# Kernel tuning notes

Hardware: AMD Instinct MI355X
Metric: run time of the kernel (lower is better)

Reference implementation:

```python
import jax, jax.numpy as jnp
import numpy as np

N = 200000
D = 256          # d_node
H = 1024         # n_hidden
OUT = 4002       # n_out
L = 2001
G = 4096         # number of graphs (static)


def _linear_params(key, fan_in, fan_out):
    kw, kb = jax.random.split(key)
    s = 1.0 / np.sqrt(fan_in)
    W = jax.random.uniform(kw, (fan_in, fan_out), jnp.float32, -s, s)
    b = jax.random.uniform(kb, (fan_out,), jnp.float32, -s, s)
    return W, b


def setup_inputs() -> dict:
    key = jax.random.key(0)
    ks = jax.random.split(key, 6)
    h = jax.random.normal(ks[0], (N, D), dtype=jnp.float32)
    node_graph_index = jnp.sort(jax.random.randint(ks[1], (N,), 0, G, dtype=jnp.int32))
    W_pool, b_pool = _linear_params(ks[2], D, D)
    W1, b1 = _linear_params(ks[3], D, H)
    W2, b2 = _linear_params(ks[4], H, H)
    W3, b3 = _linear_params(ks[5], H, OUT)
    return {"h": h, "node_graph_index": node_graph_index,
            "W_pool": W_pool, "b_pool": b_pool,
            "W1": W1, "b1": b1, "W2": W2, "b2": b2, "W3": W3, "b3": b3}


def reference(h, node_graph_index, W_pool, b_pool, W1, b1, W2, b2, W3, b3):
    # attention logits per node: SiLU(W_pool h + b)   [N, D]
    att = jax.nn.silu(h @ W_pool + b_pool)
    # per-graph, per-feature softmax over nodes (segment softmax)
    att_max = jax.ops.segment_max(att, node_graph_index, num_segments=G)   # [G, D]
    att_exp = jnp.exp(att - att_max[node_graph_index])                     # [N, D]
    att_sum = jax.ops.segment_sum(att_exp, node_graph_index, num_segments=G)  # [G, D]
    att_norm = att_exp / jnp.maximum(att_sum[node_graph_index], 1e-12)     # [N, D]
    # attention-weighted pooling
    h_G = jax.ops.segment_sum(h * att_norm, node_graph_index, num_segments=G)  # [G, D]
    # output MLP (depth=2 hidden SiLU layers, plain last)
    x = jax.nn.silu(h_G @ W1 + b1)
    x = jax.nn.silu(x @ W2 + b2)
    out = x @ W3 + b3                                                      # [G, 4002]
    eps_imag = out[:, :L]
    eps_real = out[:, L:]
    return out, eps_imag, eps_real
```

## Files before the change

### kernel.cpp

```cpp
#include <hip/hip_runtime.h>
#include <cstdint>
#include <cstddef>

#define NN 200000
#define DD 256
#define HH 1024
#define OUTD 4002
#define LL 2001
#define GG 4096

#define ROWS_PB 128
#define STEPS 8
#define SLOTS_L 8
#define SLOTS_G 4

typedef unsigned short u16;
typedef short short8 __attribute__((ext_vector_type(8)));
typedef float f32x4 __attribute__((ext_vector_type(4)));

static __device__ __forceinline__ u16 f2bf(float f) {
  uint32_t u = __float_as_uint(f);
  uint32_t r = (u + 0x7FFFu + ((u >> 16) & 1u)) >> 16;
  return (u16)r;
}
static __device__ __forceinline__ float bf2f(u16 b) {
  return __uint_as_float(((uint32_t)b) << 16);
}

static __device__ __forceinline__ void gld_lds16(const void* g, void* l) {
  __builtin_amdgcn_global_load_lds((const __attribute__((address_space(1))) void*)g,
                                   (__attribute__((address_space(3))) void*)l,
                                   16, 0, 0);
}

static __device__ __forceinline__ void barrier_nodrain() {
  asm volatile("s_waitcnt lgkmcnt(0)" ::: "memory");
  __builtin_amdgcn_s_barrier();
  __builtin_amdgcn_sched_barrier(0);
}

__global__ __launch_bounds__(256) void transpose_bf16(const float* __restrict__ W,
                                                      u16* __restrict__ WT,
                                                      int K, int Nc) {
  __shared__ float tile[32][33];
  int nt = blockIdx.x * 32, kt = blockIdx.y * 32;
  int tx = threadIdx.x & 31, ty = threadIdx.x >> 5;
#pragma unroll
  for (int i = 0; i < 4; ++i) {
    int k = kt + ty + i * 8, n = nt + tx;
    tile[ty + i * 8][tx] = (k < K && n < Nc) ? W[(size_t)k * Nc + n] : 0.f;
  }
  __syncthreads();
#pragma unroll
  for (int i = 0; i < 4; ++i) {
    int n = nt + ty + i * 8, k = kt + tx;
    if (n < Nc && k < K) WT[(size_t)n * K + k] = f2bf(tile[tx][ty + i * 8]);
  }
}

__global__ void graph_offsets(const int* __restrict__ idx, int* __restrict__ offs) {
  int g = blockIdx.x * blockDim.x + threadIdx.x;
  if (g > GG) return;
  int lo = 0, hi = NN;
  while (lo < hi) {
    int mid = (lo + hi) >> 1;
    if (idx[mid] < g) lo = mid + 1; else hi = mid;
  }
  offs[g] = lo;
}

__global__ __launch_bounds__(512) void fused_pool(const float* __restrict__ h,
                                                  const u16* __restrict__ WT,
                                                  const float* __restrict__ bias,
                                                  const int* __restrict__ idx,
                                                  const int* __restrict__ offs,
                                                  float* __restrict__ PS_ss,
                                                  float* __restrict__ PS_ah) {
  __shared__ __align__(16) u16 At[2][16 * 256];
  __shared__ float accS[SLOTS_L * 128];
  __shared__ float accA[SLOTS_L * 128];
  __shared__ int lidx[ROWS_PB];

  const int tid = threadIdx.x;
  const int wave = tid >> 6, lane = tid & 63;
  const int rl = lane & 15, q = lane >> 4;
  const int half = blockIdx.x;
  const int chunk = blockIdx.y;
  const int halfbase = half * 128;
  const long row0 = (long)chunk * ROWS_PB;

  if (tid < ROWS_PB) {
    long r = row0 + tid;
    lidx[tid] = (r < NN) ? idx[r] : -1;
  }
  for (int i = tid; i < SLOTS_L * 128; i += 512) { accS[i] = 0.f; accA[i] = 0.f; }

  const int fl = wave * 16 + rl;
  const int f0 = halfbase + fl;
  short8 Bf0[8];
  {
    const u16* wp0 = WT + (size_t)f0 * 256 + q * 8;
#pragma unroll
    for (int k0 = 0; k0 < 8; ++k0)
      Bf0[k0] = *reinterpret_cast<const short8*>(wp0 + k0 * 32);
  }
  const float bv0 = bias[f0];

  const int tr = tid >> 5, te = (tid & 31) * 8;
  const int wbyte = tr * 512 + ((te * 2) ^ ((tr & 7) << 4));
  float4 pf0, pf1;
  auto issue = [&](int st) {
    long r = row0 + (long)st * 16 + tr;
    if (r >= NN) r = NN - 1;
    const float* p = h + r * 256 + te;
    pf0 = *reinterpret_cast<const float4*>(p);
    pf1 = *reinterpret_cast<const float4*>(p + 4);
  };
  auto commit = [&](int bufsel) {
    short8 w;
    w[0] = (short)f2bf(pf0.x); w[1] = (short)f2bf(pf0.y);
    w[2] = (short)f2bf(pf0.z); w[3] = (short)f2bf(pf0.w);
    w[4] = (short)f2bf(pf1.x); w[5] = (short)f2bf(pf1.y);
    w[6] = (short)f2bf(pf1.z); w[7] = (short)f2bf(pf1.w);
    *reinterpret_cast<short8*>((char*)&At[0][0] + bufsel * 8192 + wbyte) = w;
  };

  int afoff[8], hv0off[4];
#pragma unroll
  for (int k0 = 0; k0 < 8; ++k0)
    afoff[k0] = rl * 512 + ((k0 * 64 + q * 16) ^ ((rl & 7) << 4));
#pragma unroll
  for (int reg = 0; reg < 4; ++reg) {
    int rloc = q * 4 + reg;
    hv0off[reg] = rloc * 512 + ((f0 * 2) ^ ((rloc & 7) << 4));
  }

  issue(0);
  commit(0);
  issue(1);
  barrier_nodrain();

  const int gfirst = lidx[0];
  int cur = -1;
  float ss0 = 0.f, ah0 = 0.f;

#pragma unroll
  for (int st = 0; st < STEPS; ++st) {
    const char* Ab = (const char*)&At[0][0] + (st & 1) * 8192;
    short8 af[8];
#pragma unroll
    for (int k0 = 0; k0 < 8; ++k0)
      af[k0] = *reinterpret_cast<const short8*>(Ab + afoff[k0]);
    f32x4 acc0 = {0.f, 0.f, 0.f, 0.f};
#pragma unroll
    for (int k0 = 0; k0 < 8; ++k0)
      acc0 = __builtin_amdgcn_mfma_f32_16x16x32_bf16(af[k0], Bf0[k0], acc0, 0, 0, 0);
#pragma unroll
    for (int reg = 0; reg < 4; ++reg) {
      const int rloc = q * 4 + reg;
      const int gid = lidx[st * 16 + rloc];
      float z0 = acc0[reg] + bv0;
      float a0 = z0 / (1.f + __expf(-z0));
      float x0 = __expf(a0);
      float hv0 = bf2f(*reinterpret_cast<const u16*>(Ab + hv0off[reg]));
      if (gid != cur) {
        if (cur >= 0) {
          int sl = cur - gfirst; if (sl >= SLOTS_L) sl = SLOTS_L - 1;
          atomicAdd(&accS[sl * 128 + fl], ss0);
          atomicAdd(&accA[sl * 128 + fl], ah0);
        }
        ss0 = ah0 = 0.f;
        cur = gid;
      }
      if (gid >= 0) {
        ss0 += x0;
        ah0 = __builtin_fmaf(x0, hv0, ah0);
      }
    }
    if (st + 1 < STEPS) {
      commit((st + 1) & 1);
      if (st + 2 < STEPS) issue(st + 2);
    }
    barrier_nodrain();
  }

  if (cur >= 0) {
    int sl = cur - gfirst; if (sl >= SLOTS_L) sl = SLOTS_L - 1;
    atomicAdd(&accS[sl * 128 + fl], ss0);
    atomicAdd(&accA[sl * 128 + fl], ah0);
  }
  __syncthreads();

  long lastrow = row0 + ROWS_PB - 1; if (lastrow >= NN) lastrow = NN - 1;
  const int glast = idx[lastrow];
  int gspan = glast - gfirst + 1; if (gspan > SLOTS_L) gspan = SLOTS_L;
  const int f = tid & 127, which = (tid >> 7) & 1;
  for (int s = tid >> 8; s < gspan; s += 2) {
    int g = gfirst + s;
    int osl = chunk - (offs[g] >> 7);
    if (osl < 0) osl = 0;
    if (osl >= SLOTS_G) osl = SLOTS_G - 1;
    float v = which ? accA[s * 128 + f] : accS[s * 128 + f];
    float* dst = which ? PS_ah : PS_ss;
    dst[((size_t)g * SLOTS_G + osl) * 256 + halfbase + f] = v;
  }
}

__global__ __launch_bounds__(256) void finalize_pool(const float* __restrict__ PS_ss,
                                                     const float* __restrict__ PS_ah,
                                                     const int* __restrict__ offs,
                                                     u16* __restrict__ hG) {
  int i = blockIdx.x * 256 + threadIdx.x;
  int g = i >> 8, f = i & 255;
  int s0 = offs[g], s1 = offs[g + 1];
  float o = 0.f;
  if (s1 > s0) {
    int b0 = s0 >> 7, b1 = (s1 - 1) >> 7;
    int nsl = b1 - b0 + 1; if (nsl > SLOTS_G) nsl = SLOTS_G;
    float ss = 0.f, ah = 0.f;
    for (int s = 0; s < nsl; ++s) {
      ss += PS_ss[((size_t)g * SLOTS_G + s) * 256 + f];
      ah += PS_ah[((size_t)g * SLOTS_G + s) * 256 + f];
    }
    o = ah / fmaxf(ss, 1e-12f);
  }
  hG[i] = f2bf(o);
}

template <int SILU, int MODE, int BK>
__global__ __launch_bounds__(512) void gemm_bt(const u16* __restrict__ A,
                                               const u16* __restrict__ BT,
                                               const float* __restrict__ bias,
                                               u16* __restrict__ Cb,
                                               float* __restrict__ Cf,
                                               float* __restrict__ Ci,
                                               float* __restrict__ Cr,
                                               int M, int Nn, int K) {
  constexpr int NSUB = BK / 32;
  __shared__ __align__(16) u16 As[2][NSUB][128 * 32];
  __shared__ __align__(16) u16 Bs[2][NSUB][128 * 32];
  const int tid = threadIdx.x;
  const int wave = tid >> 6, lane = tid & 63;
  const int wr = wave >> 2, wc = wave & 3;
  const long bm = (long)blockIdx.y * 128;
  const long bn = (long)blockIdx.x * 128;

  const f32x4 zero = {0.f, 0.f, 0.f, 0.f};
  f32x4 acc[4][2];
#pragma unroll
  for (int i = 0; i < 4; ++i)
#pragma unroll
    for (int j = 0; j < 2; ++j) acc[i][j] = zero;

  const int rg = lane >> 2;
  const int kc = (lane & 3) * 8;
  const int rl = lane & 15;
  const int kk = (lane >> 4) * 8;
  const int rbase = wave * 16;
  const int nt = K / BK;

  auto stage = [&](int t, int buf) {
    const long k0 = (long)t * BK;
#pragma unroll
    for (int s = 0; s < NSUB; ++s) {
      long rA = bm + rbase + rg; if (rA >= M) rA = M - 1;
      long rB = bn + rbase + rg; if (rB >= Nn) rB = Nn - 1;
      gld_lds16(A + rA * K + k0 + s * 32 + kc, &As[buf][s][rbase * 32]);
      gld_lds16(BT + rB * K + k0 + s * 32 + kc, &Bs[buf][s][rbase * 32]);
    }
  };

  stage(0, 0);
  for (int t = 0; t < nt; ++t) {
    const int buf = t & 1;
    if (t + 1 < nt) {
      stage(t + 1, buf ^ 1);
      if constexpr (NSUB == 1) {
        asm volatile("s_waitcnt vmcnt(2)" ::: "memory");
      } else {
        asm volatile("s_waitcnt vmcnt(4)" ::: "memory");
      }
    } else {
      asm volatile("s_waitcnt vmcnt(0)" ::: "memory");
    }
    __builtin_amdgcn_s_barrier();
    __builtin_amdgcn_sched_barrier(0);

#pragma unroll
    for (int s = 0; s < NSUB; ++s) {
      short8 af[4], bfr[2];
#pragma unroll
      for (int mi = 0; mi < 4; ++mi)
        af[mi] = *reinterpret_cast<const short8*>(&As[buf][s][(wr * 64 + mi * 16 + rl) * 32 + kk]);
#pragma unroll
      for (int ni = 0; ni < 2; ++ni)
        bfr[ni] = *reinterpret_cast<const short8*>(&Bs[buf][s][(wc * 32 + ni * 16 + rl) * 32 + kk]);
#pragma unroll
      for (int mi = 0; mi < 4; ++mi)
#pragma unroll
        for (int ni = 0; ni < 2; ++ni)
          acc[mi][ni] = __builtin_amdgcn_mfma_f32_16x16x32_bf16(af[mi], bfr[ni], acc[mi][ni], 0, 0, 0);
    }

    asm volatile("s_waitcnt lgkmcnt(0)" ::: "memory");
    __builtin_amdgcn_s_barrier();
    __builtin_amdgcn_sched_barrier(0);
  }

#pragma unroll
  for (int ni = 0; ni < 2; ++ni) {
    long ccol = bn + wc * 32 + ni * 16 + rl;
    if (ccol >= Nn) continue;
    float bv = bias[ccol];
#pragma unroll
    for (int mi = 0; mi < 4; ++mi) {
#pragma unroll
      for (int reg = 0; reg < 4; ++reg) {
        long rrow = bm + wr * 64 + mi * 16 + (lane >> 4) * 4 + reg;
        if (rrow >= M) continue;
        float v = acc[mi][ni][reg] + bv;
        if (SILU) v = v / (1.f + __expf(-v));
        if (MODE == 0) {
          Cb[rrow * Nn + ccol] = f2bf(v);
        } else {
          Cf[rrow * (long)OUTD + ccol] = v;
          if (ccol < LL) Ci[rrow * (long)LL + ccol] = v;
          else           Cr[rrow * (long)LL + (ccol - LL)] = v;
        }
      }
    }
  }
}

extern "C" void kernel_launch(void* const* d_in, const int* in_sizes, int n_in,
                              void* d_out, int out_size, void* d_ws, size_t ws_size,
                              hipStream_t stream) {
  const float* h      = (const float*)d_in[0];
  const int*   idx    = (const int*)d_in[1];
  const float* W_pool = (const float*)d_in[2];
  const float* b_pool = (const float*)d_in[3];
  const float* W1     = (const float*)d_in[4];
  const float* b1     = (const float*)d_in[5];
  const float* W2     = (const float*)d_in[6];
  const float* b2     = (const float*)d_in[7];
  const float* W3     = (const float*)d_in[8];
  const float* b3     = (const float*)d_in[9];

  float* out   = (float*)d_out;
  float* out_i = out + (size_t)GG * OUTD;
  float* out_r = out_i + (size_t)GG * LL;

  char* ws = (char*)d_ws;
  size_t off = 0;
  auto alloc = [&](size_t bytes) {
    void* p = ws + off;
    off += (bytes + 255) & ~(size_t)255;
    return p;
  };
  u16* WpoolT = (u16*)alloc((size_t)DD * DD * 2);
  u16* W1T    = (u16*)alloc((size_t)HH * DD * 2);
  u16* W2T    = (u16*)alloc((size_t)HH * HH * 2);
  u16* W3T    = (u16*)alloc((size_t)OUTD * HH * 2);
  u16* hG     = (u16*)alloc((size_t)GG * DD * 2);
  u16* x1     = (u16*)alloc((size_t)GG * HH * 2);
  u16* x2     = (u16*)alloc((size_t)GG * HH * 2);
  int* offs   = (int*)alloc((GG + 1) * sizeof(int));
  float* PS_ss = (float*)alloc((size_t)GG * SLOTS_G * 256 * 4);
  float* PS_ah = (float*)alloc((size_t)GG * SLOTS_G * 256 * 4);

  transpose_bf16<<<dim3(8, 8), 256, 0, stream>>>(W_pool, WpoolT, DD, DD);
  transpose_bf16<<<dim3(32, 8), 256, 0, stream>>>(W1, W1T, DD, HH);
  transpose_bf16<<<dim3(32, 32), 256, 0, stream>>>(W2, W2T, HH, HH);
  transpose_bf16<<<dim3(126, 32), 256, 0, stream>>>(W3, W3T, HH, OUTD);
  graph_offsets<<<(GG + 256) / 256, 256, 0, stream>>>(idx, offs);

  fused_pool<<<dim3(2, (NN + ROWS_PB - 1) / ROWS_PB), 512, 0, stream>>>(
      h, WpoolT, b_pool, idx, offs, PS_ss, PS_ah);
  finalize_pool<<<GG, 256, 0, stream>>>(PS_ss, PS_ah, offs, hG);

  gemm_bt<1, 0, 64><<<dim3(8, 32), 512, 0, stream>>>(
      hG, W1T, b1, x1, nullptr, nullptr, nullptr, GG, HH, DD);
  gemm_bt<1, 0, 64><<<dim3(8, 32), 512, 0, stream>>>(
      x1, W2T, b2, x2, nullptr, nullptr, nullptr, GG, HH, HH);
  gemm_bt<0, 1, 32><<<dim3(32, 32), 512, 0, stream>>>(
      x2, W3T, b3, nullptr, out, out_i, out_r, GG, OUTD, HH);
}
```

Baseline: 309.3 us.

## Merge feature halves into one 1024-thread block with triple-buffered row prefetch

The pooling kernel no longer splits the 256 output features across two blocks. A single 1024-thread block now covers all features for a 128-row chunk, so each h row is read from global memory once instead of twice. The prefetch pipeline becomes a 3-deep register ring feeding a 4-buffer LDS ring, and the per-block graph slot count doubles. The cost is larger LDS use and higher register pressure at 1024 threads, which may reduce occupancy.

```diff
diff --git a/kernel.cpp b/kernel.cpp
--- a/kernel.cpp
+++ b/kernel.cpp
@@ -11,11 +11,12 @@
 
 #define ROWS_PB 128
 #define STEPS 8
-#define SLOTS_L 8
+#define SLOTS_L 16
 #define SLOTS_G 4
 
 typedef unsigned short u16;
 typedef short short8 __attribute__((ext_vector_type(8)));
+typedef short short4v __attribute__((ext_vector_type(4)));
 typedef float f32x4 __attribute__((ext_vector_type(4)));
 
 static __device__ __forceinline__ u16 f2bf(float f) {
@@ -69,75 +70,69 @@
   offs[g] = lo;
 }
 
-__global__ __launch_bounds__(512) void fused_pool(const float* __restrict__ h,
-                                                  const u16* __restrict__ WT,
-                                                  const float* __restrict__ bias,
-                                                  const int* __restrict__ idx,
-                                                  const int* __restrict__ offs,
-                                                  float* __restrict__ PS_ss,
-                                                  float* __restrict__ PS_ah) {
-  __shared__ __align__(16) u16 At[2][16 * 256];
-  __shared__ float accS[SLOTS_L * 128];
-  __shared__ float accA[SLOTS_L * 128];
+__global__ __launch_bounds__(1024, 4) void fused_pool(const float* __restrict__ h,
+                                                      const u16* __restrict__ WT,
+                                                      const float* __restrict__ bias,
+                                                      const int* __restrict__ idx,
+                                                      const int* __restrict__ offs,
+                                                      float* __restrict__ PS_ss,
+                                                      float* __restrict__ PS_ah) {
+  __shared__ __align__(16) u16 At[6][16 * 256];
+  __shared__ float accS[SLOTS_L * 256];
+  __shared__ float accA[SLOTS_L * 256];
   __shared__ int lidx[ROWS_PB];
 
   const int tid = threadIdx.x;
   const int wave = tid >> 6, lane = tid & 63;
   const int rl = lane & 15, q = lane >> 4;
-  const int half = blockIdx.x;
-  const int chunk = blockIdx.y;
-  const int halfbase = half * 128;
-  const long row0 = (long)chunk * ROWS_PB;
+  const int b = blockIdx.x;
+  const long row0 = (long)b * ROWS_PB;
 
   if (tid < ROWS_PB) {
     long r = row0 + tid;
     lidx[tid] = (r < NN) ? idx[r] : -1;
   }
-  for (int i = tid; i < SLOTS_L * 128; i += 512) { accS[i] = 0.f; accA[i] = 0.f; }
-
-  const int fl = wave * 16 + rl;
-  const int f0 = halfbase + fl;
-  short8 Bf0[8];
+  for (int i = tid; i < SLOTS_L * 256; i += 1024) { accS[i] = 0.f; accA[i] = 0.f; }
+
+  const int f0 = wave * 16 + rl;
+  short8 Bf[8];
   {
-    const u16* wp0 = WT + (size_t)f0 * 256 + q * 8;
+    const u16* wp = WT + (size_t)f0 * 256 + q * 8;
 #pragma unroll
     for (int k0 = 0; k0 < 8; ++k0)
-      Bf0[k0] = *reinterpret_cast<const short8*>(wp0 + k0 * 32);
+      Bf[k0] = *reinterpret_cast<const short8*>(wp + k0 * 32);
   }
   const float bv0 = bias[f0];
 
-  const int tr = tid >> 5, te = (tid & 31) * 8;
+  const int tr = wave, te = lane * 4;
   const int wbyte = tr * 512 + ((te * 2) ^ ((tr & 7) << 4));
-  float4 pf0, pf1;
-  auto issue = [&](int st) {
+  float4 pf[3];
+  auto issue = [&](int st, int slot) {
     long r = row0 + (long)st * 16 + tr;
     if (r >= NN) r = NN - 1;
-    const float* p = h + r * 256 + te;
-    pf0 = *reinterpret_cast<const float4*>(p);
-    pf1 = *reinterpret_cast<const float4*>(p + 4);
+    pf[slot] = *reinterpret_cast<const float4*>(h + r * 256 + te);
   };
-  auto commit = [&](int bufsel) {
-    short8 w;
-    w[0] = (short)f2bf(pf0.x); w[1] = (short)f2bf(pf0.y);
-    w[2] = (short)f2bf(pf0.z); w[3] = (short)f2bf(pf0.w);
-    w[4] = (short)f2bf(pf1.x); w[5] = (short)f2bf(pf1.y);
-    w[6] = (short)f2bf(pf1.z); w[7] = (short)f2bf(pf1.w);
-    *reinterpret_cast<short8*>((char*)&At[0][0] + bufsel * 8192 + wbyte) = w;
+  auto commit = [&](int st, int slot) {
+    short4v w;
+    w[0] = (short)f2bf(pf[slot].x); w[1] = (short)f2bf(pf[slot].y);
+    w[2] = (short)f2bf(pf[slot].z); w[3] = (short)f2bf(pf[slot].w);
+    *reinterpret_cast<short4v*>((char*)&At[st & 3][0] + wbyte) = w;
   };
 
-  int afoff[8], hv0off[4];
+  int afoff[8], hvoff[4];
 #pragma unroll
   for (int k0 = 0; k0 < 8; ++k0)
     afoff[k0] = rl * 512 + ((k0 * 64 + q * 16) ^ ((rl & 7) << 4));
 #pragma unroll
   for (int reg = 0; reg < 4; ++reg) {
     int rloc = q * 4 + reg;
-    hv0off[reg] = rloc * 512 + ((f0 * 2) ^ ((rloc & 7) << 4));
-  }
-
-  issue(0);
-  commit(0);
-  issue(1);
+    hvoff[reg] = rloc * 512 + ((f0 * 2) ^ ((rloc & 7) << 4));
+  }
+
+  issue(0, 0);
+  issue(1, 1);
+  issue(2, 2);
+  commit(0, 0);
   barrier_nodrain();
 
   const int gfirst = lidx[0];
@@ -146,7 +141,7 @@
 
 #pragma unroll
   for (int st = 0; st < STEPS; ++st) {
-    const char* Ab = (const char*)&At[0][0] + (st & 1) * 8192;
+    const char* Ab = (const char*)&At[st & 3][0];
     short8 af[8];
 #pragma unroll
     for (int k0 = 0; k0 < 8; ++k0)
@@ -154,7 +149,7 @@
     f32x4 acc0 = {0.f, 0.f, 0.f, 0.f};
 #pragma unroll
     for (int k0 = 0; k0 < 8; ++k0)
-      acc0 = __builtin_amdgcn_mfma_f32_16x16x32_bf16(af[k0], Bf0[k0], acc0, 0, 0, 0);
+      acc0 = __builtin_amdgcn_mfma_f32_16x16x32_bf16(af[k0], Bf[k0], acc0, 0, 0, 0);
 #pragma unroll
     for (int reg = 0; reg < 4; ++reg) {
       const int rloc = q * 4 + reg;
@@ -162,12 +157,12 @@
       float z0 = acc0[reg] + bv0;
       float a0 = z0 / (1.f + __expf(-z0));
       float x0 = __expf(a0);
-      float hv0 = bf2f(*reinterpret_cast<const u16*>(Ab + hv0off[reg]));
+      float hv0 = bf2f(*reinterpret_cast<const u16*>(Ab + hvoff[reg]));
       if (gid != cur) {
         if (cur >= 0) {
           int sl = cur - gfirst; if (sl >= SLOTS_L) sl = SLOTS_L - 1;
-          atomicAdd(&accS[sl * 128 + fl], ss0);
-          atomicAdd(&accA[sl * 128 + fl], ah0);
+          atomicAdd(&accS[sl * 256 + f0], ss0);
+          atomicAdd(&accA[sl * 256 + f0], ah0);
         }
         ss0 = ah0 = 0.f;
         cur = gid;
@@ -177,32 +172,30 @@
         ah0 = __builtin_fmaf(x0, hv0, ah0);
       }
     }
-    if (st + 1 < STEPS) {
-      commit((st + 1) & 1);
-      if (st + 2 < STEPS) issue(st + 2);
-    }
+    if (st + 1 < STEPS) commit(st + 1, (st + 1) % 3);
+    if (st + 3 < STEPS) issue(st + 3, st % 3);
     barrier_nodrain();
   }
 
   if (cur >= 0) {
     int sl = cur - gfirst; if (sl >= SLOTS_L) sl = SLOTS_L - 1;
-    atomicAdd(&accS[sl * 128 + fl], ss0);
-    atomicAdd(&accA[sl * 128 + fl], ah0);
+    atomicAdd(&accS[sl * 256 + f0], ss0);
+    atomicAdd(&accA[sl * 256 + f0], ah0);
   }
   __syncthreads();
 
   long lastrow = row0 + ROWS_PB - 1; if (lastrow >= NN) lastrow = NN - 1;
   const int glast = idx[lastrow];
   int gspan = glast - gfirst + 1; if (gspan > SLOTS_L) gspan = SLOTS_L;
-  const int f = tid & 127, which = (tid >> 7) & 1;
-  for (int s = tid >> 8; s < gspan; s += 2) {
+  const int f = tid & 255, which = (tid >> 8) & 1;
+  for (int s = tid >> 9; s < gspan; s += 2) {
     int g = gfirst + s;
-    int osl = chunk - (offs[g] >> 7);
+    int osl = b - (offs[g] >> 7);
     if (osl < 0) osl = 0;
     if (osl >= SLOTS_G) osl = SLOTS_G - 1;
-    float v = which ? accA[s * 128 + f] : accS[s * 128 + f];
+    float v = which ? accA[s * 256 + f] : accS[s * 256 + f];
     float* dst = which ? PS_ah : PS_ss;
-    dst[((size_t)g * SLOTS_G + osl) * 256 + halfbase + f] = v;
+    dst[((size_t)g * SLOTS_G + osl) * 256 + f] = v;
   }
 }
 
@@ -374,7 +367,7 @@
   transpose_bf16<<<dim3(126, 32), 256, 0, stream>>>(W3, W3T, HH, OUTD);
   graph_offsets<<<(GG + 256) / 256, 256, 0, stream>>>(idx, offs);
 
-  fused_pool<<<dim3(2, (NN + ROWS_PB - 1) / ROWS_PB), 512, 0, stream>>>(
+  fused_pool<<<(NN + ROWS_PB - 1) / ROWS_PB, 1024, 0, stream>>>(
       h, WpoolT, b_pool, idx, offs, PS_ss, PS_ah);
   finalize_pool<<<GG, 256, 0, stream>>>(PS_ss, PS_ah, offs, hG);
 
```

Result: slower. 330.8 us (+6.9%).
